# Kernel optimization log

Measured on AMD Instinct MI355X. Metric: run time of the kernel, lower is better.

The kernel has to match this reference:

```python
import jax, jax.numpy as jnp
import numpy as np

EPS = 1e-5
RATIO = 8


def _conv3d(x, w, b, groups=1, pad=0):
    # x: [N,C,T,H,W], w: [O, C//groups, kT,kH,kW]
    y = jax.lax.conv_general_dilated(
        x, w, window_strides=(1, 1, 1), padding=[(pad, pad)] * 3,
        dimension_numbers=("NCDHW", "OIDHW", "NCDHW"), feature_group_count=groups)
    return y + b[None, :, None, None, None]


def _dwblock(x, pw1_w, pw1_b, dw_w, dw_b, pw2_w, pw2_b):
    # pointwise1 (1x1x1) -> depthwise 3x3x3 -> pointwise2 (1x1x1)
    mid = pw1_w.shape[0]
    x = _conv3d(x, pw1_w, pw1_b)
    x = _conv3d(x, dw_w, dw_b, groups=mid, pad=1)
    x = _conv3d(x, pw2_w, pw2_b)
    return x


def _make_dw_params(key, c_in, c_out, prefix):
    mid = c_in // RATIO
    ks = jax.random.split(key, 3)
    s = 0.02
    return {
        f"{prefix}_pw1_w": jax.random.normal(ks[0], (mid, c_in, 1, 1, 1), jnp.float32) * s,
        f"{prefix}_pw1_b": jnp.zeros((mid,), jnp.float32),
        f"{prefix}_dw_w": jax.random.normal(ks[1], (mid, 1, 3, 3, 3), jnp.float32) * s,
        f"{prefix}_dw_b": jnp.zeros((mid,), jnp.float32),
        f"{prefix}_pw2_w": jax.random.normal(ks[2], (c_out, mid, 1, 1, 1), jnp.float32) * s,
        f"{prefix}_pw2_b": jnp.zeros((c_out,), jnp.float32),
    }


def setup_inputs() -> dict:
    key = jax.random.key(0)
    N, C, T, H, W = 4, 256, 16, 28, 28
    KC, VC = 128, 256
    k0, k1, k2, k3, k4 = jax.random.split(key, 5)
    inp = {"input_": jax.random.normal(k0, (N, C, T, H, W), jnp.float32)}
    inp.update(_make_dw_params(k1, C, KC, "k"))
    inp.update(_make_dw_params(k2, C, KC, "q"))
    inp.update(_make_dw_params(k3, C, VC, "v"))
    inp.update(_make_dw_params(k4, VC, C, "r"))
    return inp


HEAD_COUNT = 8


def reference(input_,
              k_pw1_w, k_pw1_b, k_dw_w, k_dw_b, k_pw2_w, k_pw2_b,
              q_pw1_w, q_pw1_b, q_dw_w, q_dw_b, q_pw2_w, q_pw2_b,
              v_pw1_w, v_pw1_b, v_dw_w, v_dw_b, v_pw2_w, v_pw2_b,
              r_pw1_w, r_pw1_b, r_dw_w, r_dw_b, r_pw2_w, r_pw2_b):
    n, c, t, h, w = input_.shape
    L = t * h * w
    Hc = HEAD_COUNT

    keys = _dwblock(input_, k_pw1_w, k_pw1_b, k_dw_w, k_dw_b, k_pw2_w, k_pw2_b)
    queries = _dwblock(input_, q_pw1_w, q_pw1_b, q_dw_w, q_dw_b, q_pw2_w, q_pw2_b)
    values = _dwblock(input_, v_pw1_w, v_pw1_b, v_dw_w, v_dw_b, v_pw2_w, v_pw2_b)

    kc = keys.shape[1]
    vc = values.shape[1]
    hk, hv = kc // Hc, vc // Hc

    # [n, heads, head_dim, L]
    K = keys.reshape(n, Hc, hk, L)
    Q = queries.reshape(n, Hc, hk, L)
    V = values.reshape(n, Hc, hv, L)

    K = jax.nn.softmax(K, axis=3)          # softmax over sequence (dim=2 in torch slice)
    Q = jax.nn.softmax(Q, axis=2)          # softmax over per-head key channels (dim=1)

    # context = K @ V^T : [n, heads, hk, hv]
    context = jnp.einsum("nhkl,nhvl->nhkv", K, V)
    # attended = context^T @ Q : [n, heads, hv, L]
    attended = jnp.einsum("nhkv,nhkl->nhvl", context, Q)
    aggregated = attended.reshape(n, vc, t, h, w)

    reproj = _dwblock(aggregated, r_pw1_w, r_pw1_b, r_dw_w, r_dw_b, r_pw2_w, r_pw2_b)
    x = reproj + input_
    # f.layer_norm(x, x.size()): normalize over the WHOLE tensor, no affine
    mu = jnp.mean(x)
    var = jnp.mean((x - mu) ** 2)
    return (x - mu) / jnp.sqrt(var + EPS)
```

## Files before the change

kernel.cpp:

```cpp
#include <hip/hip_runtime.h>
#include <cstddef>

#define NB   4
#define CIN  256
#define TT   16
#define HH   28
#define WW   28
#define LL   12544
#define MIDC 32
#define KCC  128
#define VCC  256
#define HC   8
#define HK   16
#define HV   32
#define CTXSPLIT 14
#define CTXSTR 544
#define EPSV 1e-5f

typedef __attribute__((ext_vector_type(8))) short bf16x8;
typedef __attribute__((ext_vector_type(8))) unsigned short u16x8;
typedef __attribute__((ext_vector_type(4))) float f32x4;
typedef __attribute__((ext_vector_type(4))) unsigned short u16x4;

__device__ __forceinline__ float b2f(unsigned short u) {
    return __builtin_bit_cast(float, ((unsigned int)u) << 16);
}
__device__ __forceinline__ unsigned short f2b(float f) {
    unsigned int u = __builtin_bit_cast(unsigned int, f);
    u += 0x7FFFu + ((u >> 16) & 1u);
    return (unsigned short)(u >> 16);
}

#define XTF_N_STRIDE 3211264ull
#define MID_SET_STRIDE 1605632ull

struct WconvA { const float* w1[4]; const float* w2[4]; };
struct Pw1M  { const short* wt[3]; const float* b[3]; unsigned short* out[3]; };
struct DwA   { const unsigned short* in[3]; const float* w[3]; const float* b[3]; unsigned short* out[3]; };
struct Pw2M  { const short* w2f; const unsigned short* d; const float* b[3]; unsigned short* out[3]; };

__global__ __launch_bounds__(256) void wconv_kernel(WconvA a, short* __restrict__ w1f,
                                                    short* __restrict__ w2f)
{
    const int g = blockIdx.x*256 + threadIdx.x;
    if (g < 4096) {
        const int L = g & 63, kap = (g >> 6) & 7, mt = (g >> 9) & 1, set = g >> 10;
        const int m = 16*mt + (L & 15);
        const int c0 = 32*kap + 8*(L >> 4);
        const float* wp = a.w1[set] + m*CIN + c0;
#pragma unroll
        for (int j = 0; j < 8; ++j) w1f[(size_t)g*8 + j] = (short)f2b(wp[j]);
    } else if (g < 4096 + 3072) {
        const int g2 = g - 4096;
        const int L = g2 & 63, mtg = g2 >> 6;
        int set, mtl;
        if (mtg < 8)       { set = 0; mtl = mtg; }
        else if (mtg < 16) { set = 1; mtl = mtg - 8; }
        else if (mtg < 32) { set = 2; mtl = mtg - 16; }
        else               { set = 3; mtl = mtg - 32; }
        const int m = 16*mtl + (L & 15);
        const int c0 = 8*(L >> 4);
        const float* wp = a.w2[set] + m*MIDC + c0;
#pragma unroll
        for (int j = 0; j < 8; ++j) w2f[(size_t)g2*8 + j] = (short)f2b(wp[j]);
    }
}

__global__ __launch_bounds__(128) void pw1_direct2(const float* __restrict__ in, Pw1M a)
{
    const int n = blockIdx.y;
    const int t = threadIdx.x, wid = t >> 6, lane = t & 63;
    const int tau = blockIdx.x*2 + wid;
    const float* ib = in + (size_t)n*CIN*LL;
    const int colb = lane & 15, qq = lane >> 4;

    f32x4 acc[3][2];
#pragma unroll
    for (int s = 0; s < 3; ++s)
#pragma unroll
        for (int mt = 0; mt < 2; ++mt)
#pragma unroll
            for (int r = 0; r < 4; ++r) acc[s][mt][r] = 0.f;

    for (int kap = 0; kap < 8; ++kap) {
        const int c0 = 32*kap + 8*qq;
        const float* p = ib + (size_t)c0*LL + tau*16 + colb;
        bf16x8 bfr;
#pragma unroll
        for (int j = 0; j < 8; ++j) bfr[j] = (short)f2b(p[(size_t)j*LL]);
#pragma unroll
        for (int s = 0; s < 3; ++s) {
#pragma unroll
            for (int mt = 0; mt < 2; ++mt) {
                bf16x8 afr = *reinterpret_cast<const bf16x8*>(
                    a.wt[s] + ((mt*8 + kap)*512 + lane*8));
                acc[s][mt] = __builtin_amdgcn_mfma_f32_16x16x32_bf16(afr, bfr, acc[s][mt], 0, 0, 0);
            }
        }
    }
#pragma unroll
    for (int s = 0; s < 3; ++s) {
        const float* bb = a.b[s];
        unsigned short* op = a.out[s] + (size_t)n*MIDC*LL;
#pragma unroll
        for (int mt = 0; mt < 2; ++mt) {
            const int m0 = mt*16 + qq*4;
#pragma unroll
            for (int r = 0; r < 4; ++r)
                op[(size_t)(m0 + r)*LL + tau*16 + colb] = f2b(acc[s][mt][r] + bb[m0 + r]);
        }
    }
}

__global__ __launch_bounds__(256) void pw1_frag(const short* __restrict__ xtf, Pw1M a)
{
    const int n = blockIdx.y, bx = blockIdx.x;
    const int t = threadIdx.x, wid = t >> 6, lane = t & 63;
    const int mt = wid & 1, lh = wid >> 1;
    const int tau0 = bx*8 + lh*4;
    const short* xb = xtf + (size_t)n*XTF_N_STRIDE;

    f32x4 acc[4];
#pragma unroll
    for (int i = 0; i < 4; ++i)
#pragma unroll
        for (int r = 0; r < 4; ++r) acc[i][r] = 0.f;

    for (int kap = 0; kap < 8; ++kap) {
        bf16x8 afr = *reinterpret_cast<const bf16x8*>(a.wt[0] + ((mt*8 + kap)*512 + lane*8));
#pragma unroll
        for (int i = 0; i < 4; ++i) {
            bf16x8 bfr = *reinterpret_cast<const bf16x8*>(
                xb + ((size_t)((tau0 + i)*8 + kap)*512 + lane*8));
            acc[i] = __builtin_amdgcn_mfma_f32_16x16x32_bf16(afr, bfr, acc[i], 0, 0, 0);
        }
    }
    const float* bb = a.b[0];
    unsigned short* op = a.out[0] + (size_t)n*MIDC*LL;
    const int col = lane & 15;
    const int m0 = mt*16 + (lane >> 4)*4;
#pragma unroll
    for (int r = 0; r < 4; ++r) {
        const float bv = bb[m0 + r];
#pragma unroll
        for (int i = 0; i < 4; ++i)
            op[(size_t)(m0 + r)*LL + (tau0 + i)*16 + col] = f2b(acc[i][r] + bv);
    }
}

struct Row6 { float v[6]; };

__device__ __forceinline__ Row6 load_row(const unsigned short* base, int zz, int yy, int x0)
{
    Row6 r;
    const bool ok = (zz >= 0) && (zz < TT) && (yy >= 0) && (yy < HH);
    if (ok) {
        const unsigned short* p = base + zz*(HH*WW) + yy*WW + x0;
        u16x4 m4 = *reinterpret_cast<const u16x4*>(p);
        r.v[0] = (x0 > 0)  ? b2f(p[-1]) : 0.f;
        r.v[1] = b2f(m4[0]); r.v[2] = b2f(m4[1]);
        r.v[3] = b2f(m4[2]); r.v[4] = b2f(m4[3]);
        r.v[5] = (x0 < 24) ? b2f(p[4]) : 0.f;
    } else {
#pragma unroll
        for (int i = 0; i < 6; ++i) r.v[i] = 0.f;
    }
    return r;
}

__device__ __forceinline__ void acc9(float& a0, float& a1, float& a2, float& a3,
                                     const Row6* rows, const float* w9)
{
#pragma unroll
    for (int dy = 0; dy < 3; ++dy)
#pragma unroll
        for (int dx = 0; dx < 3; ++dx) {
            const float wv = w9[dy*3 + dx];
            a0 = fmaf(wv, rows[dy].v[0 + dx], a0);
            a1 = fmaf(wv, rows[dy].v[1 + dx], a1);
            a2 = fmaf(wv, rows[dy].v[2 + dx], a2);
            a3 = fmaf(wv, rows[dy].v[3 + dx], a3);
        }
}

__global__ __launch_bounds__(256) void dw_reg(DwA a)
{
    const int tid = threadIdx.x;
    if (tid >= 196) return;
    const int z  = blockIdx.z;
    const int nm = blockIdx.y;
    const int m  = nm & (MIDC-1);
    const int t0 = blockIdx.x * 8;

    const float* wp = a.w[z] + m*27;
    float wv[27];
#pragma unroll
    for (int i = 0; i < 27; ++i) wv[i] = wp[i];
    const float bias = a.b[z][m];

    const int xg = tid % 7, y = tid / 7;
    const int x0 = xg*4;
    const unsigned short* ip = a.in[z] + (size_t)nm*LL;
    unsigned short* op = a.out[z] + (size_t)nm*LL;

    Row6 win[3][3];
#pragma unroll
    for (int dy = 0; dy < 3; ++dy) {
        win[0][dy] = load_row(ip, t0-1, y+dy-1, x0);
        win[1][dy] = load_row(ip, t0,   y+dy-1, x0);
    }
#pragma unroll
    for (int tt = 0; tt < 8; ++tt) {
        const int p0 = tt % 3, p1 = (tt+1) % 3, p2 = (tt+2) % 3;
        const int znew = t0 + tt + 1;
        win[p2][0] = load_row(ip, znew, y-1, x0);
        win[p2][1] = load_row(ip, znew, y,   x0);
        win[p2][2] = load_row(ip, znew, y+1, x0);

        float a0 = bias, a1 = bias, a2 = bias, a3 = bias;
        acc9(a0, a1, a2, a3, win[p0], wv);
        acc9(a0, a1, a2, a3, win[p1], wv + 9);
        acc9(a0, a1, a2, a3, win[p2], wv + 18);

        u16x4 o4 = { f2b(a0), f2b(a1), f2b(a2), f2b(a3) };
        *reinterpret_cast<u16x4*>(op + (size_t)(t0+tt)*(HH*WW) + y*WW + x0) = o4;
    }
}

__global__ __launch_bounds__(256) void pw2_g(Pw2M a)
{
    const int z = blockIdx.z, n = blockIdx.y, bx = blockIdx.x;
    int set, chunk;
    if (z < 2)      { set = 0; chunk = z; }
    else if (z < 4) { set = 1; chunk = z - 2; }
    else            { set = 2; chunk = z - 4; }
    const int OC   = (set == 2) ? 256 : 128;
    const int off2 = (set == 0) ? 0 : (set == 1) ? 8 : 16;

    const int t = threadIdx.x, wid = t >> 6, lane = t & 63;
    const int mtile = chunk*4 + wid;
    bf16x8 afr = *reinterpret_cast<const bf16x8*>(
        a.w2f + ((size_t)(off2 + mtile)*512 + lane*8));
    const unsigned short* db = a.d + (size_t)set*MID_SET_STRIDE + (size_t)n*MIDC*LL;
    const int colb = lane & 15, c0 = 8*(lane >> 4);

    f32x4 acc[4];
#pragma unroll
    for (int i = 0; i < 4; ++i) {
#pragma unroll
        for (int r = 0; r < 4; ++r) acc[i][r] = 0.f;
        const unsigned short* p = db + (size_t)c0*LL + (bx*4 + i)*16 + colb;
        bf16x8 bfr;
#pragma unroll
        for (int j = 0; j < 8; ++j) bfr[j] = (short)p[(size_t)j*LL];
        acc[i] = __builtin_amdgcn_mfma_f32_16x16x32_bf16(afr, bfr, acc[i], 0, 0, 0);
    }
    const float* bb = a.b[set];
    unsigned short* op = a.out[set] + (size_t)n*OC*LL;
    const int m0 = 16*mtile + (lane >> 4)*4;
#pragma unroll
    for (int r = 0; r < 4; ++r) {
        const float bv = bb[m0 + r];
#pragma unroll
        for (int i = 0; i < 4; ++i)
            op[(size_t)(m0 + r)*LL + (bx*4 + i)*16 + colb] = f2b(acc[i][r] + bv);
    }
}

__global__ __launch_bounds__(256) void ctx_mfma(
    const unsigned short* __restrict__ Kb, const unsigned short* __restrict__ Vb,
    float* __restrict__ ctxp)
{
    const int nh = blockIdx.y;
    const int sp = blockIdx.x;
    const int n = nh >> 3, h = nh & 7;
    const int t = threadIdx.x, w = t >> 6, lane = t & 63;
    const int i = lane & 15, q = lane >> 4;

    const unsigned short* Kp = Kb + ((size_t)(n*KCC + h*HK))*LL;
    const unsigned short* Vp = Vb + ((size_t)(n*VCC + h*HV))*LL;

    f32x4 a0 = {0.f,0.f,0.f,0.f}, a1 = {0.f,0.f,0.f,0.f};
    float asum = 0.f;

    const int cbase = sp*28 + w*7;
#pragma unroll 2
    for (int cc = 0; cc < 7; ++cc) {
        const int l0 = (cbase + cc)*32 + 8*q;
        bf16x8 kf = *reinterpret_cast<const bf16x8*>(Kp + (size_t)i*LL + l0);
        bf16x8 pf;
#pragma unroll
        for (int j = 0; j < 8; ++j) {
            const float e = __expf(b2f((unsigned short)kf[j]));
            asum += e;
            pf[j] = (short)f2b(e);
        }
        bf16x8 b0 = *reinterpret_cast<const bf16x8*>(Vp + (size_t)i*LL + l0);
        bf16x8 b1 = *reinterpret_cast<const bf16x8*>(Vp + (size_t)(i+16)*LL + l0);
        a0 = __builtin_amdgcn_mfma_f32_16x16x32_bf16(pf, b0, a0, 0, 0, 0);
        a1 = __builtin_amdgcn_mfma_f32_16x16x32_bf16(pf, b1, a1, 0, 0, 0);
    }
    asum += __shfl_xor(asum, 16);
    asum += __shfl_xor(asum, 32);

    __shared__ float cs[4][512];
    __shared__ float as[4][16];
#pragma unroll
    for (int r = 0; r < 4; ++r) {
        cs[w][(q*4 + r)*32 + i]      = a0[r];
        cs[w][(q*4 + r)*32 + 16 + i] = a1[r];
    }
    if (q == 0) as[w][i] = asum;
    __syncthreads();
    float* cp = ctxp + ((size_t)nh*CTXSPLIT + sp)*CTXSTR;
    for (int p = t; p < 512; p += 256)
        cp[p] = cs[0][p] + cs[1][p] + cs[2][p] + cs[3][p];
    if (t < 16) cp[512 + t] = as[0][t] + as[1][t] + as[2][t] + as[3][t];
}

__global__ void ctx_reduce(const float* __restrict__ ctxp, float* __restrict__ ctx)
{
    const int idx = blockIdx.x*256 + threadIdx.x;
    const int nh = idx >> 9;
    const int p  = idx & 511;
    const int k  = p >> 5;
    float s = 0.f, se = 0.f;
    for (int sp = 0; sp < CTXSPLIT; ++sp) {
        const float* cp = ctxp + ((size_t)nh*CTXSPLIT + sp)*CTXSTR;
        s  += cp[p];
        se += cp[512 + k];
    }
    ctx[idx] = s / se;
}

__global__ __launch_bounds__(256) void attended_kernel(
    const float* __restrict__ ctx, const unsigned short* __restrict__ Qb,
    short* __restrict__ aggf)
{
    const int nh = blockIdx.y;
    const int n = nh >> 3, h = nh & 7;
    const int l = blockIdx.x*256 + threadIdx.x;
    const float* __restrict__ cl = ctx + (size_t)nh*512;

    const unsigned short* Qp = Qb + ((size_t)(n*KCC + h*HK))*LL + l;
    float q[HK];
    float mx = -1e30f;
#pragma unroll
    for (int k = 0; k < HK; ++k) { q[k] = b2f(Qp[(size_t)k*LL]); mx = fmaxf(mx, q[k]); }
    float s = 0.f;
#pragma unroll
    for (int k = 0; k < HK; ++k) { q[k] = __expf(q[k] - mx); s += q[k]; }
    const float inv = 1.f / s;
#pragma unroll
    for (int k = 0; k < HK; ++k) q[k] *= inv;

    float av[HV];
#pragma unroll 4
    for (int v = 0; v < HV; ++v) {
        float acc = 0.f;
#pragma unroll
        for (int k = 0; k < HK; ++k) acc += q[k] * cl[k*HV + v];
        av[v] = acc;
    }
    short* ob = aggf + (size_t)n*XTF_N_STRIDE + ((size_t)((l >> 4)*8 + h))*512;
#pragma unroll
    for (int qd = 0; qd < 4; ++qd) {
        bf16x8 vv;
#pragma unroll
        for (int j = 0; j < 8; ++j) vv[j] = (short)f2b(av[qd*8 + j]);
        *reinterpret_cast<bf16x8*>(ob + (qd*16 + (l & 15))*8) = vv;
    }
}

__global__ __launch_bounds__(256) void pw2r_g(
    const unsigned short* __restrict__ d, const short* __restrict__ w2f,
    const float* __restrict__ bias, const float* __restrict__ resid,
    unsigned short* __restrict__ xout, float* __restrict__ part)
{
    const int z = blockIdx.z, n = blockIdx.y, bx = blockIdx.x;
    const int t = threadIdx.x, wid = t >> 6, lane = t & 63;
    const int mtile = z*4 + wid;
    bf16x8 afr = *reinterpret_cast<const bf16x8*>(
        w2f + ((size_t)(32 + mtile)*512 + lane*8));
    const unsigned short* db = d + (size_t)n*MIDC*LL;
    const int colb = lane & 15, c0 = 8*(lane >> 4);

    f32x4 acc[4];
#pragma unroll
    for (int i = 0; i < 4; ++i) {
#pragma unroll
        for (int r = 0; r < 4; ++r) acc[i][r] = 0.f;
        const unsigned short* p = db + (size_t)c0*LL + (bx*4 + i)*16 + colb;
        bf16x8 bfr;
#pragma unroll
        for (int j = 0; j < 8; ++j) bfr[j] = (short)p[(size_t)j*LL];
        acc[i] = __builtin_amdgcn_mfma_f32_16x16x32_bf16(afr, bfr, acc[i], 0, 0, 0);
    }
    const int m0 = 16*mtile + (lane >> 4)*4;
    float s1 = 0.f, s2 = 0.f;
#pragma unroll
    for (int r = 0; r < 4; ++r) {
        const float bv = bias[m0 + r];
#pragma unroll
        for (int i = 0; i < 4; ++i) {
            const size_t off = (size_t)(n*CIN + m0 + r)*LL + (bx*4 + i)*16 + colb;
            const float v = acc[i][r] + bv + resid[off];
            xout[off] = f2b(v);
            s1 += v; s2 += v*v;
        }
    }
    __shared__ float red[256];
    const int bid = (z*NB + n)*196 + bx;
    red[t] = s1; __syncthreads();
    for (int s = 128; s > 0; s >>= 1) { if (t < s) red[t] += red[t+s]; __syncthreads(); }
    if (t == 0) part[2*bid] = red[0];
    __syncthreads();
    red[t] = s2; __syncthreads();
    for (int s = 128; s > 0; s >>= 1) { if (t < s) red[t] += red[t+s]; __syncthreads(); }
    if (t == 0) part[2*bid + 1] = red[0];
}

__global__ void stats_kernel(const float* __restrict__ part, int nblocks,
                             float* __restrict__ stats)
{
    __shared__ float r1[256], r2[256];
    const int t = threadIdx.x;
    float s1 = 0.f, s2 = 0.f;
    for (int i = t; i < nblocks; i += 256) { s1 += part[2*i]; s2 += part[2*i+1]; }
    r1[t] = s1; r2[t] = s2; __syncthreads();
    for (int s = 128; s > 0; s >>= 1) { if (t < s) { r1[t] += r1[t+s]; r2[t] += r2[t+s]; } __syncthreads(); }
    if (t == 0) {
        const float M = (float)NB*CIN*LL;
        const float mu = r1[0]/M;
        const float var = r2[0]/M - mu*mu;
        stats[0] = mu;
        stats[1] = 1.0f/sqrtf(var + EPSV);
    }
}

__global__ __launch_bounds__(256) void norm_bf16(
    const unsigned short* __restrict__ x, const float* __restrict__ stats,
    float* __restrict__ out)
{
    const float mu = stats[0], inv = stats[1];
    const size_t total = (size_t)NB*CIN*LL;
    for (size_t i = ((size_t)blockIdx.x*256 + threadIdx.x)*8; i < total;
         i += (size_t)gridDim.x*256*8) {
        u16x8 v = *reinterpret_cast<const u16x8*>(x + i);
        float4 o0, o1;
        o0.x = (b2f(v[0])-mu)*inv; o0.y = (b2f(v[1])-mu)*inv;
        o0.z = (b2f(v[2])-mu)*inv; o0.w = (b2f(v[3])-mu)*inv;
        o1.x = (b2f(v[4])-mu)*inv; o1.y = (b2f(v[5])-mu)*inv;
        o1.z = (b2f(v[6])-mu)*inv; o1.w = (b2f(v[7])-mu)*inv;
        *reinterpret_cast<float4*>(out + i)     = o0;
        *reinterpret_cast<float4*>(out + i + 4) = o1;
    }
}

extern "C" void kernel_launch(void* const* d_in, const int* in_sizes, int n_in,
                              void* d_out, int out_size, void* d_ws, size_t ws_size,
                              hipStream_t stream) {
    const float* input   = (const float*)d_in[0];
    const float* k_pw1_w = (const float*)d_in[1];
    const float* k_pw1_b = (const float*)d_in[2];
    const float* k_dw_w  = (const float*)d_in[3];
    const float* k_dw_b  = (const float*)d_in[4];
    const float* k_pw2_w = (const float*)d_in[5];
    const float* k_pw2_b = (const float*)d_in[6];
    const float* q_pw1_w = (const float*)d_in[7];
    const float* q_pw1_b = (const float*)d_in[8];
    const float* q_dw_w  = (const float*)d_in[9];
    const float* q_dw_b  = (const float*)d_in[10];
    const float* q_pw2_w = (const float*)d_in[11];
    const float* q_pw2_b = (const float*)d_in[12];
    const float* v_pw1_w = (const float*)d_in[13];
    const float* v_pw1_b = (const float*)d_in[14];
    const float* v_dw_w  = (const float*)d_in[15];
    const float* v_dw_b  = (const float*)d_in[16];
    const float* v_pw2_w = (const float*)d_in[17];
    const float* v_pw2_b = (const float*)d_in[18];
    const float* r_pw1_w = (const float*)d_in[19];
    const float* r_pw1_b = (const float*)d_in[20];
    const float* r_dw_w  = (const float*)d_in[21];
    const float* r_dw_b  = (const float*)d_in[22];
    const float* r_pw2_w = (const float*)d_in[23];
    const float* r_pw2_b = (const float*)d_in[24];

    char* base = (char*)d_ws;
    unsigned short* dbuf = (unsigned short*)base;
    short* aggf = (short*)base;
    unsigned short* midb  = (unsigned short*)(base + 25690112);
    unsigned short* mid_r = midb;
    unsigned short* d_r   = (unsigned short*)(base + 25690112 + 6422528);
    unsigned short* Kb = (unsigned short*)(base + 54591488);
    unsigned short* Qb = (unsigned short*)(base + 67436544);
    unsigned short* Vb = (unsigned short*)(base + 80281600);
    unsigned short* xb = (unsigned short*)(base + 54591488);
    char* H = base + 105971712;
    float* ctxp   = (float*)H;
    float* ctx    = (float*)(H + 974848);
    float* part   = (float*)(H + 1040384);
    float* statsp = (float*)(H + 1065472);
    short* w1f    = (short*)(H + 1065536);
    short* w2f    = (short*)(H + 1131072);

    {
        WconvA a;
        a.w1[0]=k_pw1_w; a.w1[1]=q_pw1_w; a.w1[2]=v_pw1_w; a.w1[3]=r_pw1_w;
        a.w2[0]=k_pw2_w; a.w2[1]=q_pw2_w; a.w2[2]=v_pw2_w; a.w2[3]=r_pw2_w;
        wconv_kernel<<<28, 256, 0, stream>>>(a, w1f, w2f);
    }
    {
        Pw1M a;
        a.wt[0]=w1f;        a.wt[1]=w1f+8192;   a.wt[2]=w1f+16384;
        a.b[0]=k_pw1_b;     a.b[1]=q_pw1_b;     a.b[2]=v_pw1_b;
        a.out[0]=midb;      a.out[1]=midb+MID_SET_STRIDE; a.out[2]=midb+2*MID_SET_STRIDE;
        pw1_direct2<<<dim3(392, NB), 128, 0, stream>>>(input, a);
    }
    {
        DwA a;
        a.in[0]=midb; a.in[1]=midb+MID_SET_STRIDE; a.in[2]=midb+2*MID_SET_STRIDE;
        a.w[0]=k_dw_w; a.w[1]=q_dw_w; a.w[2]=v_dw_w;
        a.b[0]=k_dw_b; a.b[1]=q_dw_b; a.b[2]=v_dw_b;
        a.out[0]=dbuf; a.out[1]=dbuf+MID_SET_STRIDE; a.out[2]=dbuf+2*MID_SET_STRIDE;
        dw_reg<<<dim3(2, NB*MIDC, 3), 256, 0, stream>>>(a);
    }
    {
        Pw2M a;
        a.w2f = w2f; a.d = dbuf;
        a.b[0]=k_pw2_b; a.b[1]=q_pw2_b; a.b[2]=v_pw2_b;
        a.out[0]=Kb; a.out[1]=Qb; a.out[2]=Vb;
        pw2_g<<<dim3(196, NB, 8), 256, 0, stream>>>(a);
    }
    ctx_mfma<<<dim3(CTXSPLIT, NB*HC), 256, 0, stream>>>(Kb, Vb, ctxp);
    ctx_reduce<<<64, 256, 0, stream>>>(ctxp, ctx);
    attended_kernel<<<dim3(49, NB*HC), 256, 0, stream>>>(ctx, Qb, aggf);
    {
        Pw1M a;
        a.wt[0]=w1f+24576; a.wt[1]=a.wt[0]; a.wt[2]=a.wt[0];
        a.b[0]=r_pw1_b;    a.b[1]=a.b[0];   a.b[2]=a.b[0];
        a.out[0]=mid_r;    a.out[1]=a.out[0]; a.out[2]=a.out[0];
        pw1_frag<<<dim3(98, NB), 256, 0, stream>>>(aggf, a);
    }
    {
        DwA a;
        a.in[0]=mid_r; a.w[0]=r_dw_w; a.b[0]=r_dw_b; a.out[0]=d_r;
        a.in[1]=a.in[0]; a.w[1]=a.w[0]; a.b[1]=a.b[0]; a.out[1]=a.out[0];
        a.in[2]=a.in[0]; a.w[2]=a.w[0]; a.b[2]=a.b[0]; a.out[2]=a.out[0];
        dw_reg<<<dim3(2, NB*MIDC, 1), 256, 0, stream>>>(a);
    }
    pw2r_g<<<dim3(196, NB, 4), 256, 0, stream>>>(d_r, w2f, r_pw2_b, input, xb, part);
    stats_kernel<<<1, 256, 0, stream>>>(part, 3136, statsp);
    norm_bf16<<<2048, 256, 0, stream>>>(xb, statsp, (float*)d_out);
}
```

Measured before the change: 143.0 us.

## Stage pw1 input tile in LDS with vectorized loads and two tiles per wave

Replaces the pw1 kernel, which gathered eight strided scalar fp32 loads per lane, with one that loads a 64-position by 256-channel input tile using float4 reads. It converts the tile to bf16 and transposes it into padded shared memory, and MFMA B fragments are then read as 16-byte LDS vectors. Each wave now processes two 16-column tiles and reuses each weight fragment across both, which halves the grid and the weight fetches. The costs are about 33KB of LDS per block, which lowers occupancy, and a block-wide sync.

```diff
diff --git a/kernel.cpp b/kernel.cpp
--- a/kernel.cpp
+++ b/kernel.cpp
@@ -16,6 +16,7 @@
 #define CTXSPLIT 14
 #define CTXSTR 544
 #define EPSV 1e-5f
+#define XPAD 264
 
 typedef __attribute__((ext_vector_type(8))) short bf16x8;
 typedef __attribute__((ext_vector_type(8))) unsigned short u16x8;
@@ -66,35 +67,60 @@
     }
 }
 
-__global__ __launch_bounds__(128) void pw1_direct2(const float* __restrict__ in, Pw1M a)
-{
+__global__ __launch_bounds__(128) void pw1_lds(const float* __restrict__ in, Pw1M a)
+{
+    __shared__ unsigned short xs[64*XPAD];
     const int n = blockIdx.y;
+    const int l0 = blockIdx.x*64;
     const int t = threadIdx.x, wid = t >> 6, lane = t & 63;
-    const int tau = blockIdx.x*2 + wid;
     const float* ib = in + (size_t)n*CIN*LL;
+
+    const int lt = (t & 15)*4;
+    const int cp = (t >> 4)*2;
+#pragma unroll 4
+    for (int cc = 0; cc < 16; ++cc) {
+        const int c = cc*16 + cp;
+        float4 va = *reinterpret_cast<const float4*>(ib + (size_t)c*LL + l0 + lt);
+        float4 vb = *reinterpret_cast<const float4*>(ib + (size_t)(c+1)*LL + l0 + lt);
+        unsigned int p0 = (unsigned int)f2b(va.x) | ((unsigned int)f2b(vb.x) << 16);
+        unsigned int p1 = (unsigned int)f2b(va.y) | ((unsigned int)f2b(vb.y) << 16);
+        unsigned int p2 = (unsigned int)f2b(va.z) | ((unsigned int)f2b(vb.z) << 16);
+        unsigned int p3 = (unsigned int)f2b(va.w) | ((unsigned int)f2b(vb.w) << 16);
+        *reinterpret_cast<unsigned int*>(&xs[(lt+0)*XPAD + c]) = p0;
+        *reinterpret_cast<unsigned int*>(&xs[(lt+1)*XPAD + c]) = p1;
+        *reinterpret_cast<unsigned int*>(&xs[(lt+2)*XPAD + c]) = p2;
+        *reinterpret_cast<unsigned int*>(&xs[(lt+3)*XPAD + c]) = p3;
+    }
+    __syncthreads();
+
     const int colb = lane & 15, qq = lane >> 4;
-
-    f32x4 acc[3][2];
+    f32x4 acc[3][2][2];
 #pragma unroll
     for (int s = 0; s < 3; ++s)
 #pragma unroll
         for (int mt = 0; mt < 2; ++mt)
 #pragma unroll
-            for (int r = 0; r < 4; ++r) acc[s][mt][r] = 0.f;
+            for (int ti = 0; ti < 2; ++ti)
+#pragma unroll
+                for (int r = 0; r < 4; ++r) acc[s][mt][ti][r] = 0.f;
 
     for (int kap = 0; kap < 8; ++kap) {
-        const int c0 = 32*kap + 8*qq;
-        const float* p = ib + (size_t)c0*LL + tau*16 + colb;
-        bf16x8 bfr;
-#pragma unroll
-        for (int j = 0; j < 8; ++j) bfr[j] = (short)f2b(p[(size_t)j*LL]);
+        bf16x8 bfr[2];
+#pragma unroll
+        for (int ti = 0; ti < 2; ++ti) {
+            const int ll = (wid*2 + ti)*16 + colb;
+            bfr[ti] = *reinterpret_cast<const bf16x8*>(&xs[ll*XPAD + kap*32 + 8*qq]);
+        }
 #pragma unroll
         for (int s = 0; s < 3; ++s) {
 #pragma unroll
             for (int mt = 0; mt < 2; ++mt) {
                 bf16x8 afr = *reinterpret_cast<const bf16x8*>(
                     a.wt[s] + ((mt*8 + kap)*512 + lane*8));
-                acc[s][mt] = __builtin_amdgcn_mfma_f32_16x16x32_bf16(afr, bfr, acc[s][mt], 0, 0, 0);
+#pragma unroll
+                for (int ti = 0; ti < 2; ++ti)
+                    acc[s][mt][ti] = __builtin_amdgcn_mfma_f32_16x16x32_bf16(
+                        afr, bfr[ti], acc[s][mt][ti], 0, 0, 0);
             }
         }
     }
@@ -106,8 +132,12 @@
         for (int mt = 0; mt < 2; ++mt) {
             const int m0 = mt*16 + qq*4;
 #pragma unroll
-            for (int r = 0; r < 4; ++r)
-                op[(size_t)(m0 + r)*LL + tau*16 + colb] = f2b(acc[s][mt][r] + bb[m0 + r]);
+            for (int ti = 0; ti < 2; ++ti) {
+                const int lg = l0 + (wid*2 + ti)*16 + colb;
+#pragma unroll
+                for (int r = 0; r < 4; ++r)
+                    op[(size_t)(m0 + r)*LL + lg] = f2b(acc[s][mt][ti][r] + bb[m0 + r]);
+            }
         }
     }
 }
@@ -515,7 +545,7 @@
         a.wt[0]=w1f;        a.wt[1]=w1f+8192;   a.wt[2]=w1f+16384;
         a.b[0]=k_pw1_b;     a.b[1]=q_pw1_b;     a.b[2]=v_pw1_b;
         a.out[0]=midb;      a.out[1]=midb+MID_SET_STRIDE; a.out[2]=midb+2*MID_SET_STRIDE;
-        pw1_direct2<<<dim3(392, NB), 128, 0, stream>>>(input, a);
+        pw1_lds<<<dim3(196, NB), 128, 0, stream>>>(input, a);
     }
     {
         DwA a;
```

After: 143.5 us. About the same (+0.3%).

## Fuse attended computation with reprojection pointwise1 via shared-memory tile

Applied to the files above, without the earlier changes.

Merges the attended kernel (Q softmax times context) and the reprojection pointwise-1 MFMA GEMM into one kernel. Each block computes the 256-channel aggregated tile for 128 positions into padded LDS and immediately runs the 256->32 MFMA from it. This removes the global write and re-read of the aggregated bf16 tensor and one launch. In exchange the grid drops to 392 blocks with about 66KB of LDS each, which lowers occupancy, and each thread does four serial softmax/context phases.

```diff
diff --git a/kernel.cpp b/kernel.cpp
--- a/kernel.cpp
+++ b/kernel.cpp
@@ -16,6 +16,7 @@
 #define CTXSPLIT 14
 #define CTXSTR 544
 #define EPSV 1e-5f
+#define APAD 264
 
 typedef __attribute__((ext_vector_type(8))) short bf16x8;
 typedef __attribute__((ext_vector_type(8))) unsigned short u16x8;
@@ -31,7 +32,6 @@
     return (unsigned short)(u >> 16);
 }
 
-#define XTF_N_STRIDE 3211264ull
 #define MID_SET_STRIDE 1605632ull
 
 struct WconvA { const float* w1[4]; const float* w2[4]; };
@@ -112,42 +112,6 @@
     }
 }
 
-__global__ __launch_bounds__(256) void pw1_frag(const short* __restrict__ xtf, Pw1M a)
-{
-    const int n = blockIdx.y, bx = blockIdx.x;
-    const int t = threadIdx.x, wid = t >> 6, lane = t & 63;
-    const int mt = wid & 1, lh = wid >> 1;
-    const int tau0 = bx*8 + lh*4;
-    const short* xb = xtf + (size_t)n*XTF_N_STRIDE;
-
-    f32x4 acc[4];
-#pragma unroll
-    for (int i = 0; i < 4; ++i)
-#pragma unroll
-        for (int r = 0; r < 4; ++r) acc[i][r] = 0.f;
-
-    for (int kap = 0; kap < 8; ++kap) {
-        bf16x8 afr = *reinterpret_cast<const bf16x8*>(a.wt[0] + ((mt*8 + kap)*512 + lane*8));
-#pragma unroll
-        for (int i = 0; i < 4; ++i) {
-            bf16x8 bfr = *reinterpret_cast<const bf16x8*>(
-                xb + ((size_t)((tau0 + i)*8 + kap)*512 + lane*8));
-            acc[i] = __builtin_amdgcn_mfma_f32_16x16x32_bf16(afr, bfr, acc[i], 0, 0, 0);
-        }
-    }
-    const float* bb = a.b[0];
-    unsigned short* op = a.out[0] + (size_t)n*MIDC*LL;
-    const int col = lane & 15;
-    const int m0 = mt*16 + (lane >> 4)*4;
-#pragma unroll
-    for (int r = 0; r < 4; ++r) {
-        const float bv = bb[m0 + r];
-#pragma unroll
-        for (int i = 0; i < 4; ++i)
-            op[(size_t)(m0 + r)*LL + (tau0 + i)*16 + col] = f2b(acc[i][r] + bv);
-    }
-}
-
 struct Row6 { float v[6]; };
 
 __device__ __forceinline__ Row6 load_row(const unsigned short* base, int zz, int yy, int x0)
@@ -333,42 +297,90 @@
     ctx[idx] = s / se;
 }
 
-__global__ __launch_bounds__(256) void attended_kernel(
-    const float* __restrict__ ctx, const unsigned short* __restrict__ Qb,
-    short* __restrict__ aggf)
-{
-    const int nh = blockIdx.y;
-    const int n = nh >> 3, h = nh & 7;
-    const int l = blockIdx.x*256 + threadIdx.x;
-    const float* __restrict__ cl = ctx + (size_t)nh*512;
-
-    const unsigned short* Qp = Qb + ((size_t)(n*KCC + h*HK))*LL + l;
-    float q[HK];
-    float mx = -1e30f;
-#pragma unroll
-    for (int k = 0; k < HK; ++k) { q[k] = b2f(Qp[(size_t)k*LL]); mx = fmaxf(mx, q[k]); }
-    float s = 0.f;
-#pragma unroll
-    for (int k = 0; k < HK; ++k) { q[k] = __expf(q[k] - mx); s += q[k]; }
-    const float inv = 1.f / s;
-#pragma unroll
-    for (int k = 0; k < HK; ++k) q[k] *= inv;
-
-    float av[HV];
+__global__ __launch_bounds__(256) void att_pw1r(
+    const unsigned short* __restrict__ Qb, const float* __restrict__ ctx,
+    const short* __restrict__ w1fr, const float* __restrict__ b1r,
+    unsigned short* __restrict__ mid_r)
+{
+    __shared__ short aggt[128*APAD];
+    const int n = blockIdx.y, bx = blockIdx.x;
+    const int t = threadIdx.x;
+    const int l0 = bx*128;
+
+    for (int ph = 0; ph < 4; ++ph) {
+        const int id = ph*256 + t;
+        const int l = id & 127, h = id >> 7;
+        const int nh = n*HC + h;
+        const unsigned short* Qp = Qb + ((size_t)(n*KCC + h*HK))*LL + l0 + l;
+        float q[HK];
+        float mx = -1e30f;
+#pragma unroll
+        for (int k = 0; k < HK; ++k) { q[k] = b2f(Qp[(size_t)k*LL]); mx = fmaxf(mx, q[k]); }
+        float s = 0.f;
+#pragma unroll
+        for (int k = 0; k < HK; ++k) { q[k] = __expf(q[k] - mx); s += q[k]; }
+        const float inv = 1.f / s;
+#pragma unroll
+        for (int k = 0; k < HK; ++k) q[k] *= inv;
+
+        const float* __restrict__ cl = ctx + (size_t)nh*512;
+        float av[HV];
 #pragma unroll 4
-    for (int v = 0; v < HV; ++v) {
-        float acc = 0.f;
-#pragma unroll
-        for (int k = 0; k < HK; ++k) acc += q[k] * cl[k*HV + v];
-        av[v] = acc;
-    }
-    short* ob = aggf + (size_t)n*XTF_N_STRIDE + ((size_t)((l >> 4)*8 + h))*512;
-#pragma unroll
-    for (int qd = 0; qd < 4; ++qd) {
-        bf16x8 vv;
-#pragma unroll
-        for (int j = 0; j < 8; ++j) vv[j] = (short)f2b(av[qd*8 + j]);
-        *reinterpret_cast<bf16x8*>(ob + (qd*16 + (l & 15))*8) = vv;
+        for (int v = 0; v < HV; ++v) {
+            float acc = 0.f;
+#pragma unroll
+            for (int k = 0; k < HK; ++k) acc += q[k] * cl[k*HV + v];
+            av[v] = acc;
+        }
+        short* row = &aggt[l*APAD + h*32];
+#pragma unroll
+        for (int qd = 0; qd < 4; ++qd) {
+            bf16x8 vv;
+#pragma unroll
+            for (int j = 0; j < 8; ++j) vv[j] = (short)f2b(av[qd*8 + j]);
+            *reinterpret_cast<bf16x8*>(row + qd*8) = vv;
+        }
+    }
+    __syncthreads();
+
+    const int wid = t >> 6, lane = t & 63;
+    const int colb = lane & 15, qq = lane >> 4;
+    f32x4 acc[2][2];
+#pragma unroll
+    for (int mt = 0; mt < 2; ++mt)
+#pragma unroll
+        for (int ti = 0; ti < 2; ++ti)
+#pragma unroll
+            for (int r = 0; r < 4; ++r) acc[mt][ti][r] = 0.f;
+
+    for (int kap = 0; kap < 8; ++kap) {
+        bf16x8 bfr[2];
+#pragma unroll
+        for (int ti = 0; ti < 2; ++ti) {
+            const int ll = (wid*2 + ti)*16 + colb;
+            bfr[ti] = *reinterpret_cast<const bf16x8*>(&aggt[ll*APAD + kap*32 + 8*qq]);
+        }
+#pragma unroll
+        for (int mt = 0; mt < 2; ++mt) {
+            bf16x8 afr = *reinterpret_cast<const bf16x8*>(
+                w1fr + ((mt*8 + kap)*512 + lane*8));
+#pragma unroll
+            for (int ti = 0; ti < 2; ++ti)
+                acc[mt][ti] = __builtin_amdgcn_mfma_f32_16x16x32_bf16(
+                    afr, bfr[ti], acc[mt][ti], 0, 0, 0);
+        }
+    }
+    unsigned short* op = mid_r + (size_t)n*MIDC*LL;
+#pragma unroll
+    for (int mt = 0; mt < 2; ++mt) {
+        const int m0 = mt*16 + qq*4;
+#pragma unroll
+        for (int ti = 0; ti < 2; ++ti) {
+            const int lg = l0 + (wid*2 + ti)*16 + colb;
+#pragma unroll
+            for (int r = 0; r < 4; ++r)
+                op[(size_t)(m0 + r)*LL + lg] = f2b(acc[mt][ti][r] + b1r[m0 + r]);
+        }
     }
 }
 
@@ -488,7 +500,6 @@
 
     char* base = (char*)d_ws;
     unsigned short* dbuf = (unsigned short*)base;
-    short* aggf = (short*)base;
     unsigned short* midb  = (unsigned short*)(base + 25690112);
     unsigned short* mid_r = midb;
     unsigned short* d_r   = (unsigned short*)(base + 25690112 + 6422528);
@@ -534,14 +545,7 @@
     }
     ctx_mfma<<<dim3(CTXSPLIT, NB*HC), 256, 0, stream>>>(Kb, Vb, ctxp);
     ctx_reduce<<<64, 256, 0, stream>>>(ctxp, ctx);
-    attended_kernel<<<dim3(49, NB*HC), 256, 0, stream>>>(ctx, Qb, aggf);
-    {
-        Pw1M a;
-        a.wt[0]=w1f+24576; a.wt[1]=a.wt[0]; a.wt[2]=a.wt[0];
-        a.b[0]=r_pw1_b;    a.b[1]=a.b[0];   a.b[2]=a.b[0];
-        a.out[0]=mid_r;    a.out[1]=a.out[0]; a.out[2]=a.out[0];
-        pw1_frag<<<dim3(98, NB), 256, 0, stream>>>(aggf, a);
-    }
+    att_pw1r<<<dim3(98, NB), 256, 0, stream>>>(Qb, ctx, w1f + 24576, r_pw1_b, mid_r);
     {
         DwA a;
         a.in[0]=mid_r; a.w[0]=r_dw_w; a.b[0]=r_dw_b; a.out[0]=d_r;
```

New measurement: 159.3 us. +11.4%, slower.

## Restructure pw2 to reuse B fragments and fuse ctx reduction into attended

Applied to the files above, without the earlier changes.

The pw2 kernel now loads each activation fragment once per wave and multiplies it against 8 weight tiles, instead of reloading activations for every output tile. This halves the z-grid and cuts redundant strided global reads. The separate ctx_reduce launch is removed: each attended block sums the split partials into shared memory itself, and the per-k normalisation is folded into the Q scaling. This trades one kernel launch for repeated partial reduction in every attended block, and raises register use to 8 accumulators in pw2.

```diff
diff --git a/kernel.cpp b/kernel.cpp
--- a/kernel.cpp
+++ b/kernel.cpp
@@ -227,43 +227,41 @@
     }
 }
 
-__global__ __launch_bounds__(256) void pw2_g(Pw2M a)
+__global__ __launch_bounds__(256) void pw2_g2(Pw2M a)
 {
     const int z = blockIdx.z, n = blockIdx.y, bx = blockIdx.x;
-    int set, chunk;
-    if (z < 2)      { set = 0; chunk = z; }
-    else if (z < 4) { set = 1; chunk = z - 2; }
-    else            { set = 2; chunk = z - 4; }
-    const int OC   = (set == 2) ? 256 : 128;
-    const int off2 = (set == 0) ? 0 : (set == 1) ? 8 : 16;
+    const int set   = (z < 2) ? z : 2;
+    const int mbase = z * 8;
+    const int rowt0 = (z == 3) ? 8 : 0;
+    const int OC    = (set == 2) ? 256 : 128;
 
     const int t = threadIdx.x, wid = t >> 6, lane = t & 63;
-    const int mtile = chunk*4 + wid;
-    bf16x8 afr = *reinterpret_cast<const bf16x8*>(
-        a.w2f + ((size_t)(off2 + mtile)*512 + lane*8));
+    const int colb = lane & 15, qq = lane >> 4;
+    const int tau = bx*4 + wid;
+
     const unsigned short* db = a.d + (size_t)set*MID_SET_STRIDE + (size_t)n*MIDC*LL;
-    const int colb = lane & 15, c0 = 8*(lane >> 4);
-
-    f32x4 acc[4];
-#pragma unroll
-    for (int i = 0; i < 4; ++i) {
-#pragma unroll
-        for (int r = 0; r < 4; ++r) acc[i][r] = 0.f;
-        const unsigned short* p = db + (size_t)c0*LL + (bx*4 + i)*16 + colb;
-        bf16x8 bfr;
-#pragma unroll
-        for (int j = 0; j < 8; ++j) bfr[j] = (short)p[(size_t)j*LL];
-        acc[i] = __builtin_amdgcn_mfma_f32_16x16x32_bf16(afr, bfr, acc[i], 0, 0, 0);
+    const unsigned short* p = db + (size_t)(8*qq)*LL + tau*16 + colb;
+    bf16x8 bfr;
+#pragma unroll
+    for (int j = 0; j < 8; ++j) bfr[j] = (short)p[(size_t)j*LL];
+
+    f32x4 acc[8];
+#pragma unroll
+    for (int m = 0; m < 8; ++m) {
+#pragma unroll
+        for (int r = 0; r < 4; ++r) acc[m][r] = 0.f;
+        bf16x8 afr = *reinterpret_cast<const bf16x8*>(
+            a.w2f + ((size_t)(mbase + m)*512 + lane*8));
+        acc[m] = __builtin_amdgcn_mfma_f32_16x16x32_bf16(afr, bfr, acc[m], 0, 0, 0);
     }
     const float* bb = a.b[set];
     unsigned short* op = a.out[set] + (size_t)n*OC*LL;
-    const int m0 = 16*mtile + (lane >> 4)*4;
-#pragma unroll
-    for (int r = 0; r < 4; ++r) {
-        const float bv = bb[m0 + r];
-#pragma unroll
-        for (int i = 0; i < 4; ++i)
-            op[(size_t)(m0 + r)*LL + (bx*4 + i)*16 + colb] = f2b(acc[i][r] + bv);
+#pragma unroll
+    for (int m = 0; m < 8; ++m) {
+        const int m0 = 16*(rowt0 + m) + qq*4;
+#pragma unroll
+        for (int r = 0; r < 4; ++r)
+            op[(size_t)(m0 + r)*LL + tau*16 + colb] = f2b(acc[m][r] + bb[m0 + r]);
     }
 }
 
@@ -318,30 +316,32 @@
     if (t < 16) cp[512 + t] = as[0][t] + as[1][t] + as[2][t] + as[3][t];
 }
 
-__global__ void ctx_reduce(const float* __restrict__ ctxp, float* __restrict__ ctx)
-{
-    const int idx = blockIdx.x*256 + threadIdx.x;
-    const int nh = idx >> 9;
-    const int p  = idx & 511;
-    const int k  = p >> 5;
-    float s = 0.f, se = 0.f;
-    for (int sp = 0; sp < CTXSPLIT; ++sp) {
-        const float* cp = ctxp + ((size_t)nh*CTXSPLIT + sp)*CTXSTR;
-        s  += cp[p];
-        se += cp[512 + k];
-    }
-    ctx[idx] = s / se;
-}
-
-__global__ __launch_bounds__(256) void attended_kernel(
-    const float* __restrict__ ctx, const unsigned short* __restrict__ Qb,
+__global__ __launch_bounds__(256) void attended_r(
+    const float* __restrict__ ctxp, const unsigned short* __restrict__ Qb,
     short* __restrict__ aggf)
 {
+    __shared__ float cl[512];
+    __shared__ float sl[16];
     const int nh = blockIdx.y;
     const int n = nh >> 3, h = nh & 7;
-    const int l = blockIdx.x*256 + threadIdx.x;
-    const float* __restrict__ cl = ctx + (size_t)nh*512;
-
+    const int t = threadIdx.x;
+
+    const float* cp0 = ctxp + (size_t)nh*CTXSPLIT*CTXSTR;
+    for (int p = t; p < 512; p += 256) {
+        float s = 0.f;
+#pragma unroll
+        for (int sp = 0; sp < CTXSPLIT; ++sp) s += cp0[sp*CTXSTR + p];
+        cl[p] = s;
+    }
+    if (t < 16) {
+        float se = 0.f;
+#pragma unroll
+        for (int sp = 0; sp < CTXSPLIT; ++sp) se += cp0[sp*CTXSTR + 512 + t];
+        sl[t] = 1.f / se;
+    }
+    __syncthreads();
+
+    const int l = blockIdx.x*256 + t;
     const unsigned short* Qp = Qb + ((size_t)(n*KCC + h*HK))*LL + l;
     float q[HK];
     float mx = -1e30f;
@@ -352,7 +352,7 @@
     for (int k = 0; k < HK; ++k) { q[k] = __expf(q[k] - mx); s += q[k]; }
     const float inv = 1.f / s;
 #pragma unroll
-    for (int k = 0; k < HK; ++k) q[k] *= inv;
+    for (int k = 0; k < HK; ++k) q[k] *= inv * sl[k];
 
     float av[HV];
 #pragma unroll 4
@@ -498,7 +498,6 @@
     unsigned short* xb = (unsigned short*)(base + 54591488);
     char* H = base + 105971712;
     float* ctxp   = (float*)H;
-    float* ctx    = (float*)(H + 974848);
     float* part   = (float*)(H + 1040384);
     float* statsp = (float*)(H + 1065472);
     short* w1f    = (short*)(H + 1065536);
@@ -530,11 +529,10 @@
         a.w2f = w2f; a.d = dbuf;
         a.b[0]=k_pw2_b; a.b[1]=q_pw2_b; a.b[2]=v_pw2_b;
         a.out[0]=Kb; a.out[1]=Qb; a.out[2]=Vb;
-        pw2_g<<<dim3(196, NB, 8), 256, 0, stream>>>(a);
+        pw2_g2<<<dim3(196, NB, 4), 256, 0, stream>>>(a);
     }
     ctx_mfma<<<dim3(CTXSPLIT, NB*HC), 256, 0, stream>>>(Kb, Vb, ctxp);
-    ctx_reduce<<<64, 256, 0, stream>>>(ctxp, ctx);
-    attended_kernel<<<dim3(49, NB*HC), 256, 0, stream>>>(ctx, Qb, aggf);
+    attended_r<<<dim3(49, NB*HC), 256, 0, stream>>>(ctxp, Qb, aggf);
     {
         Pw1M a;
         a.wt[0]=w1f+24576; a.wt[1]=a.wt[0]; a.wt[2]=a.wt[0];
```

Measured after the change: 143.8 us. About the same (+0.5%).
